# Kernel optimization log

Hardware: AMD Instinct MI355X
Metric: run time of the kernel (lower is better)

## Reference

```python
import jax, jax.numpy as jnp
import numpy as np

NUM_EXPERTS = 8
TOP_K = 2
DIM = 1024
HIDDEN = 2048
TOKENS = 8192


def setup_inputs() -> dict:
    key = jax.random.key(0)
    k0, k1, k2, k3, k4 = jax.random.split(key, 5)
    x = jax.random.normal(k0, (TOKENS, DIM), dtype=jnp.float32)
    gate_w = jax.random.normal(k1, (NUM_EXPERTS, DIM), dtype=jnp.float32) * 0.02
    # SwiGLU expert weights, stacked over experts
    w1 = jax.random.normal(k2, (NUM_EXPERTS, DIM, HIDDEN), dtype=jnp.float32) * 0.02
    w3 = jax.random.normal(k3, (NUM_EXPERTS, DIM, HIDDEN), dtype=jnp.float32) * 0.02
    w2 = jax.random.normal(k4, (NUM_EXPERTS, HIDDEN, DIM), dtype=jnp.float32) * 0.02
    return {"x": x, "gate_w": gate_w, "w1": w1, "w3": w3, "w2": w2}


def reference(x, gate_w, w1, w3, w2):
    # x: [T, D]; gate_w: [E, D]; w1,w3: [E, D, H]; w2: [E, H, D]
    E = gate_w.shape[0]
    gate_logits = x @ gate_w.T                               # [T, E]
    topk_vals, topk_idx = jax.lax.top_k(gate_logits, TOP_K)  # [T, K]
    topk_w = jax.nn.softmax(topk_vals.astype(jnp.float32), axis=-1).astype(x.dtype)
    # per-token per-expert combine weight: sum_k w[t,k] * [sel[t,k]==e]  -> [T, E]
    combine = jnp.einsum('tk,tke->te', topk_w,
                         jax.nn.one_hot(topk_idx, E, dtype=x.dtype))
    # SwiGLU experts, computed per expert over all tokens then masked-combined
    h = jnp.einsum('td,edh->eth', x, w1)                     # [E, T, H]
    g = jnp.einsum('td,edh->eth', x, w3)                     # [E, T, H]
    y = jnp.einsum('eth,ehd->etd', jax.nn.silu(h) * g, w2)   # [E, T, D]
    return jnp.einsum('te,etd->td', combine, y)              # [T, D]
```

## Files before the change

### kernel.cpp

```cpp
#include <hip/hip_runtime.h>
#include <cstdint>
#include <cstddef>

#define T_TOKENS 8192
#define DIM      1024
#define HID      2048
#define NE       8
#define HCAP     17408

typedef __attribute__((ext_vector_type(8))) short short8;
typedef __attribute__((ext_vector_type(4))) short short4v;
typedef __attribute__((ext_vector_type(4))) float f32x4;

__device__ __forceinline__ unsigned short f2bf(float f) {
  unsigned int u = __builtin_bit_cast(unsigned int, f);
  u += 0x7fffu + ((u >> 16) & 1u);
  return (unsigned short)(u >> 16);
}

__device__ __forceinline__ void gload16(const void* g, void* lds) {
  __builtin_amdgcn_global_load_lds((const __attribute__((address_space(1))) void*)g,
                                   (__attribute__((address_space(3))) void*)lds,
                                   16, 0, 0);
}

__global__ void transcvt_kernel(const float* __restrict__ in, unsigned short* __restrict__ out,
                                int K, int N) {
  __shared__ float tile[64][65];
  int e = blockIdx.z;
  int r  = threadIdx.x >> 2;
  int c0 = (threadIdx.x & 3) * 16;
  const float* src = in + ((size_t)e * K + blockIdx.y * 64 + r) * N + blockIdx.x * 64 + c0;
#pragma unroll
  for (int j = 0; j < 4; j++) {
    float4 v = *(const float4*)(src + j * 4);
    tile[r][c0 + j * 4 + 0] = v.x; tile[r][c0 + j * 4 + 1] = v.y;
    tile[r][c0 + j * 4 + 2] = v.z; tile[r][c0 + j * 4 + 3] = v.w;
  }
  __syncthreads();
  short8 o0, o1;
#pragma unroll
  for (int j = 0; j < 8; j++) o0[j] = (short)f2bf(tile[c0 + j][r]);
#pragma unroll
  for (int j = 0; j < 8; j++) o1[j] = (short)f2bf(tile[c0 + 8 + j][r]);
  unsigned short* dst = out + ((size_t)e * N + blockIdx.x * 64 + r) * K + blockIdx.y * 64 + c0;
  *(short8*)dst = o0;
  *(short8*)(dst + 8) = o1;
}

__global__ void gate_kernel(const float* __restrict__ x, const float* __restrict__ gw,
                            int2* __restrict__ sel, float2* __restrict__ wts,
                            unsigned short* __restrict__ xb) {
  int wid = threadIdx.x >> 6, lane = threadIdx.x & 63;
  int t = blockIdx.x * 4 + wid;
  const float* xr = x + (size_t)t * DIM;
  unsigned short* xo = xb + (size_t)t * DIM;
  double acc[NE];
#pragma unroll
  for (int e = 0; e < NE; e++) acc[e] = 0.0;
#pragma unroll
  for (int p = 0; p < 4; p++) {
    int idx = p * 256 + lane * 4;
    float4 xv = *(const float4*)(xr + idx);
    short4v o;
    o[0] = (short)f2bf(xv.x); o[1] = (short)f2bf(xv.y);
    o[2] = (short)f2bf(xv.z); o[3] = (short)f2bf(xv.w);
    *(short4v*)(xo + idx) = o;
#pragma unroll
    for (int e = 0; e < NE; e++) {
      float4 g = *(const float4*)(gw + e * DIM + idx);
      acc[e] += (double)xv.x * (double)g.x + (double)xv.y * (double)g.y
              + (double)xv.z * (double)g.z + (double)xv.w * (double)g.w;
    }
  }
#pragma unroll
  for (int e = 0; e < NE; e++) {
    double v = acc[e];
#pragma unroll
    for (int off = 32; off > 0; off >>= 1) v += __shfl_xor(v, off);
    acc[e] = v;
  }
  if (lane == 0) {
    float l[NE];
#pragma unroll
    for (int e = 0; e < NE; e++) l[e] = (float)acc[e];
    int i0 = 0; float v0 = l[0];
#pragma unroll
    for (int e = 1; e < NE; e++) if (l[e] > v0) { v0 = l[e]; i0 = e; }
    int i1 = -1; float v1 = -3.4e38f;
#pragma unroll
    for (int e = 0; e < NE; e++) if (e != i0 && l[e] > v1) { v1 = l[e]; i1 = e; }
    float ew = __expf(v1 - v0);
    float w0 = 1.0f / (1.0f + ew);
    float w1 = ew / (1.0f + ew);
    sel[t] = make_int2(i0, i1);
    wts[t] = make_float2(w0, w1);
  }
}

__global__ void scatter_kernel(const int2* __restrict__ sel, const float2* __restrict__ wts,
                               int* __restrict__ cnt, int* __restrict__ btok,
                               float* __restrict__ bw) {
  __shared__ int hist[NE];
  __shared__ int base[NE];
  int tid = threadIdx.x;
  if (tid < NE) hist[tid] = 0;
  __syncthreads();
  int t = blockIdx.x * 256 + tid;
  int2 s = sel[t]; float2 w = wts[t];
  int p0 = atomicAdd(&hist[s.x], 1);
  int p1 = atomicAdd(&hist[s.y], 1);
  __syncthreads();
  if (tid < NE) base[tid] = atomicAdd(&cnt[tid], hist[tid]);
  __syncthreads();
  int o0 = base[s.x] + p0;
  btok[s.x * T_TOKENS + o0] = t; bw[s.x * T_TOKENS + o0] = w.x;
  int o1 = base[s.y] + p1;
  btok[s.y * T_TOKENS + o1] = t; bw[s.y * T_TOKENS + o1] = w.y;
}

#define G1_NT (HID / 64)
#define G1_MT 64
#define G1_NWG (G1_NT * G1_MT * NE)
__global__ __launch_bounds__(256, 2) void gemm1_kernel(
    const unsigned short* __restrict__ xb, const unsigned short* __restrict__ w1t,
    const unsigned short* __restrict__ w3t, const int* __restrict__ cnt,
    const int* __restrict__ btok, const unsigned short* __restrict__ zbuf,
    unsigned short* __restrict__ h) {
  int bid = blockIdx.x;
  int wg = (bid & 7) * (G1_NWG / 8) + (bid >> 3);
  int e  = wg / (G1_NT * G1_MT);
  int rem = wg % (G1_NT * G1_MT);
  int nt = rem / G1_MT;
  int mt = rem % G1_MT;

  int cn = cnt[e];
  int pc = (cn + 127) & ~127;
  if (mt * 128 >= pc) return;
  int hoff = 0;
#pragma unroll
  for (int i = 0; i < NE; i++) { int pi = (cnt[i] + 127) & ~127; if (i < e) hoff += pi; }

  __shared__ short8 At8[1024];
  __shared__ short8 B18[512];
  __shared__ short8 B38[512];

  int tid = threadIdx.x, wid = tid >> 6, lane = tid & 63;
  int m0 = mt * 128;

  int swzcol = ((lane & 7) ^ (lane >> 3)) * 8;

  const unsigned short* asrc[4];
#pragma unroll
  for (int rd = 0; rd < 4; rd++) {
    int row = (rd * 4 + wid) * 8 + (lane >> 3);
    int r = m0 + row;
    asrc[rd] = (r < cn) ? (xb + (size_t)btok[e * T_TOKENS + r] * DIM + swzcol)
                        : (zbuf + swzcol);
  }
  const unsigned short* b1s[2]; const unsigned short* b3s[2];
#pragma unroll
  for (int rd = 0; rd < 2; rd++) {
    int row = (rd * 4 + wid) * 8 + (lane >> 3);
    size_t o = ((size_t)e * HID + nt * 64 + row) * DIM + swzcol;
    b1s[rd] = w1t + o; b3s[rd] = w3t + o;
  }

  f32x4 zero = {0.f, 0.f, 0.f, 0.f};
  f32x4 acc1[4][2], acc3[4][2];
#pragma unroll
  for (int m = 0; m < 4; m++)
#pragma unroll
    for (int n = 0; n < 2; n++) { acc1[m][n] = zero; acc3[m][n] = zero; }

  int wr = wid >> 1, wc = wid & 1;
  const char* At = (const char*)At8;
  const char* B1 = (const char*)B18;
  const char* B3 = (const char*)B38;
  int lxor = (lane & 7) << 4;

  for (int kt = 0; kt < DIM / 64; kt++) {
    int ko = kt * 64;
#pragma unroll
    for (int rd = 0; rd < 4; rd++)
      gload16(asrc[rd] + ko, (char*)At8 + (rd * 4 + wid) * 1024);
#pragma unroll
    for (int rd = 0; rd < 2; rd++) {
      gload16(b1s[rd] + ko, (char*)B18 + (rd * 4 + wid) * 1024);
      gload16(b3s[rd] + ko, (char*)B38 + (rd * 4 + wid) * 1024);
    }
    __syncthreads();
#pragma unroll
    for (int ks = 0; ks < 2; ks++) {
      int cb = (ks * 64 + (lane >> 4) * 16) ^ lxor;
      short8 a[4], f1[2], f3[2];
#pragma unroll
      for (int m = 0; m < 4; m++)
        a[m] = *(const short8*)(At + (wr * 64 + m * 16 + (lane & 15)) * 128 + cb);
#pragma unroll
      for (int n = 0; n < 2; n++) {
        int rb = (wc * 32 + n * 16 + (lane & 15)) * 128 + cb;
        f1[n] = *(const short8*)(B1 + rb);
        f3[n] = *(const short8*)(B3 + rb);
      }
#pragma unroll
      for (int m = 0; m < 4; m++)
#pragma unroll
        for (int n = 0; n < 2; n++) {
          acc1[m][n] = __builtin_amdgcn_mfma_f32_16x16x32_bf16(a[m], f1[n], acc1[m][n], 0, 0, 0);
          acc3[m][n] = __builtin_amdgcn_mfma_f32_16x16x32_bf16(a[m], f3[n], acc3[m][n], 0, 0, 0);
        }
    }
    __syncthreads();
  }

#pragma unroll
  for (int m = 0; m < 4; m++)
#pragma unroll
    for (int n = 0; n < 2; n++) {
#pragma unroll
      for (int j = 0; j < 4; j++) {
        float s1 = acc1[m][n][j], s3 = acc3[m][n][j];
        float hv = s1 / (1.0f + __expf(-s1)) * s3;
        int row = wr * 64 + m * 16 + (lane >> 4) * 4 + j;
        int col = nt * 64 + wc * 32 + n * 16 + (lane & 15);
        h[(size_t)(hoff + m0 + row) * HID + col] = f2bf(hv);
      }
    }
}

#define G2_NT (DIM / 128)
#define G2_MT 64
#define G2_NWG (G2_NT * G2_MT * NE)
__global__ __launch_bounds__(256, 2) void gemm2_kernel(
    const unsigned short* __restrict__ h, const unsigned short* __restrict__ w2t,
    const int* __restrict__ cnt, const int* __restrict__ btok,
    const float* __restrict__ bw, float* __restrict__ out) {
  int bid = blockIdx.x;
  int wg = (bid & 7) * (G2_NWG / 8) + (bid >> 3);
  int e  = wg / (G2_NT * G2_MT);
  int rem = wg % (G2_NT * G2_MT);
  int nt = rem / G2_MT;
  int mt = rem % G2_MT;

  int cn = cnt[e];
  int pc = (cn + 127) & ~127;
  if (mt * 128 >= pc) return;
  int hoff = 0;
#pragma unroll
  for (int i = 0; i < NE; i++) { int pi = (cnt[i] + 127) & ~127; if (i < e) hoff += pi; }

  __shared__ short8 At8[1024];
  __shared__ short8 Bt8[1024];

  int tid = threadIdx.x, wid = tid >> 6, lane = tid & 63;
  int m0 = mt * 128;

  int swzcol = ((lane & 7) ^ (lane >> 3)) * 8;

  const unsigned short* as[4]; const unsigned short* bs[4];
#pragma unroll
  for (int rd = 0; rd < 4; rd++) {
    int row = (rd * 4 + wid) * 8 + (lane >> 3);
    as[rd] = h + (size_t)(hoff + m0 + row) * HID + swzcol;
    bs[rd] = w2t + ((size_t)e * DIM + nt * 128 + row) * HID + swzcol;
  }

  f32x4 zero = {0.f, 0.f, 0.f, 0.f};
  f32x4 acc[4][4];
#pragma unroll
  for (int m = 0; m < 4; m++)
#pragma unroll
    for (int n = 0; n < 4; n++) acc[m][n] = zero;

  int wr = wid >> 1, wc = wid & 1;
  const char* At = (const char*)At8;
  const char* Bt = (const char*)Bt8;
  int lxor = (lane & 7) << 4;

  for (int kt = 0; kt < HID / 64; kt++) {
    int ko = kt * 64;
#pragma unroll
    for (int rd = 0; rd < 4; rd++) {
      gload16(as[rd] + ko, (char*)At8 + (rd * 4 + wid) * 1024);
      gload16(bs[rd] + ko, (char*)Bt8 + (rd * 4 + wid) * 1024);
    }
    __syncthreads();
#pragma unroll
    for (int ks = 0; ks < 2; ks++) {
      int cb = (ks * 64 + (lane >> 4) * 16) ^ lxor;
      short8 a[4], b[4];
#pragma unroll
      for (int m = 0; m < 4; m++)
        a[m] = *(const short8*)(At + (wr * 64 + m * 16 + (lane & 15)) * 128 + cb);
#pragma unroll
      for (int n = 0; n < 4; n++)
        b[n] = *(const short8*)(Bt + (wc * 64 + n * 16 + (lane & 15)) * 128 + cb);
#pragma unroll
      for (int m = 0; m < 4; m++)
#pragma unroll
        for (int n = 0; n < 4; n++)
          acc[m][n] = __builtin_amdgcn_mfma_f32_16x16x32_bf16(a[m], b[n], acc[m][n], 0, 0, 0);
    }
    __syncthreads();
  }

#pragma unroll
  for (int m = 0; m < 4; m++)
#pragma unroll
    for (int j = 0; j < 4; j++) {
      int r = m0 + wr * 64 + m * 16 + (lane >> 4) * 4 + j;
      if (r < cn) {
        int t = btok[e * T_TOKENS + r];
        float w = bw[e * T_TOKENS + r];
        size_t ob = (size_t)t * DIM + nt * 128 + wc * 64 + (lane & 15);
#pragma unroll
        for (int n = 0; n < 4; n++)
          atomicAdd(out + ob + n * 16, w * acc[m][n][j]);
      }
    }
}

extern "C" void kernel_launch(void* const* d_in, const int* in_sizes, int n_in,
                              void* d_out, int out_size, void* d_ws, size_t ws_size,
                              hipStream_t stream) {
  const float* x  = (const float*)d_in[0];
  const float* gw = (const float*)d_in[1];
  const float* w1 = (const float*)d_in[2];
  const float* w3 = (const float*)d_in[3];
  const float* w2 = (const float*)d_in[4];
  float* out = (float*)d_out;

  char* ws = (char*)d_ws;
  unsigned short* W1T = (unsigned short*)ws;
  unsigned short* W3T = W1T + (size_t)NE * HID * DIM;
  unsigned short* W2T = W3T + (size_t)NE * HID * DIM;
  unsigned short* XB  = W2T + (size_t)NE * DIM * HID;
  unsigned short* H   = XB + (size_t)T_TOKENS * DIM;
  int*   TOK = (int*)(H + (size_t)HCAP * HID);
  float* BW  = (float*)(TOK + NE * T_TOKENS);
  int*   CNT = (int*)(BW + NE * T_TOKENS);
  unsigned short* ZBUF = (unsigned short*)(CNT + 16);
  int2*   SEL = (int2*)(ZBUF + 1024);
  float2* WTS = (float2*)(SEL + T_TOKENS);

  hipMemsetAsync(d_out, 0, (size_t)out_size * sizeof(float), stream);
  hipMemsetAsync(CNT, 0, 16 * sizeof(int) + 1024 * sizeof(unsigned short), stream);

  gate_kernel<<<T_TOKENS / 4, 256, 0, stream>>>(x, gw, SEL, WTS, XB);
  scatter_kernel<<<T_TOKENS / 256, 256, 0, stream>>>(SEL, WTS, CNT, TOK, BW);
  transcvt_kernel<<<dim3(HID / 64, DIM / 64, NE), 256, 0, stream>>>(w1, W1T, DIM, HID);
  transcvt_kernel<<<dim3(HID / 64, DIM / 64, NE), 256, 0, stream>>>(w3, W3T, DIM, HID);
  transcvt_kernel<<<dim3(DIM / 64, HID / 64, NE), 256, 0, stream>>>(w2, W2T, HID, DIM);
  gemm1_kernel<<<G1_NWG, 256, 0, stream>>>(XB, W1T, W3T, CNT, TOK, ZBUF, H);
  gemm2_kernel<<<G2_NWG, 256, 0, stream>>>(H, W2T, CNT, TOK, BW, out);
}
```

Baseline: 377.3 us.

## Fuse weight transpose-convert and gating into one prep kernel; use 3D GEMM grids

Folds the three weight transpose/bf16-convert launches and the gate kernel into a single prep_kernel whose block index selects the work, cutting launch overhead and letting all of it run concurrently. The GEMM kernels drop the bid&7-based workgroup remapping (an XCD-aware swizzle) and take expert, m-tile and n-tile directly from a 3D grid. That changes dispatch order, so blocks sharing an expert's weights may spread across XCDs and lose L2 reuse.

```diff
diff --git a/kernel.cpp b/kernel.cpp
--- a/kernel.cpp
+++ b/kernel.cpp
@@ -24,13 +24,13 @@
                                    16, 0, 0);
 }
 
-__global__ void transcvt_kernel(const float* __restrict__ in, unsigned short* __restrict__ out,
-                                int K, int N) {
-  __shared__ float tile[64][65];
-  int e = blockIdx.z;
-  int r  = threadIdx.x >> 2;
-  int c0 = (threadIdx.x & 3) * 16;
-  const float* src = in + ((size_t)e * K + blockIdx.y * 64 + r) * N + blockIdx.x * 64 + c0;
+#define PREP_GATE0 12288
+__device__ __forceinline__ void transcvt_body(
+    const float* __restrict__ in, unsigned short* __restrict__ out,
+    int K, int N, int bx, int by, int e, float (*tile)[65], int tid) {
+  int r  = tid >> 2;
+  int c0 = (tid & 3) * 16;
+  const float* src = in + ((size_t)e * K + by * 64 + r) * N + bx * 64 + c0;
 #pragma unroll
   for (int j = 0; j < 4; j++) {
     float4 v = *(const float4*)(src + j * 4);
@@ -43,16 +43,38 @@
   for (int j = 0; j < 8; j++) o0[j] = (short)f2bf(tile[c0 + j][r]);
 #pragma unroll
   for (int j = 0; j < 8; j++) o1[j] = (short)f2bf(tile[c0 + 8 + j][r]);
-  unsigned short* dst = out + ((size_t)e * N + blockIdx.x * 64 + r) * K + blockIdx.y * 64 + c0;
+  unsigned short* dst = out + ((size_t)e * N + bx * 64 + r) * K + by * 64 + c0;
   *(short8*)dst = o0;
   *(short8*)(dst + 8) = o1;
 }
 
-__global__ void gate_kernel(const float* __restrict__ x, const float* __restrict__ gw,
-                            int2* __restrict__ sel, float2* __restrict__ wts,
-                            unsigned short* __restrict__ xb) {
-  int wid = threadIdx.x >> 6, lane = threadIdx.x & 63;
-  int t = blockIdx.x * 4 + wid;
+__global__ __launch_bounds__(256) void prep_kernel(
+    const float* __restrict__ x, const float* __restrict__ gw,
+    const float* __restrict__ w1, const float* __restrict__ w3,
+    const float* __restrict__ w2,
+    unsigned short* __restrict__ W1T, unsigned short* __restrict__ W3T,
+    unsigned short* __restrict__ W2T,
+    int2* __restrict__ sel, float2* __restrict__ wts,
+    unsigned short* __restrict__ xb) {
+  __shared__ float tile[64][65];
+  int bid = blockIdx.x, tid = threadIdx.x;
+
+  if (bid < PREP_GATE0) {
+    if (bid < 4096) {
+      int t = bid;
+      transcvt_body(w1, W1T, DIM, HID, t % 32, (t / 32) % 16, t / 512, tile, tid);
+    } else if (bid < 8192) {
+      int t = bid - 4096;
+      transcvt_body(w3, W3T, DIM, HID, t % 32, (t / 32) % 16, t / 512, tile, tid);
+    } else {
+      int t = bid - 8192;
+      transcvt_body(w2, W2T, HID, DIM, t % 16, (t / 16) % 32, t / 512, tile, tid);
+    }
+    return;
+  }
+
+  int wid = tid >> 6, lane = tid & 63;
+  int t = (bid - PREP_GATE0) * 4 + wid;
   const float* xr = x + (size_t)t * DIM;
   unsigned short* xo = xb + (size_t)t * DIM;
   double acc[NE];
@@ -92,9 +114,9 @@
     for (int e = 0; e < NE; e++) if (e != i0 && l[e] > v1) { v1 = l[e]; i1 = e; }
     float ew = __expf(v1 - v0);
     float w0 = 1.0f / (1.0f + ew);
-    float w1 = ew / (1.0f + ew);
+    float w1v = ew / (1.0f + ew);
     sel[t] = make_int2(i0, i1);
-    wts[t] = make_float2(w0, w1);
+    wts[t] = make_float2(w0, w1v);
   }
 }
 
@@ -119,27 +141,20 @@
   btok[s.y * T_TOKENS + o1] = t; bw[s.y * T_TOKENS + o1] = w.y;
 }
 
-#define G1_NT (HID / 64)
-#define G1_MT 64
-#define G1_NWG (G1_NT * G1_MT * NE)
 __global__ __launch_bounds__(256, 2) void gemm1_kernel(
     const unsigned short* __restrict__ xb, const unsigned short* __restrict__ w1t,
     const unsigned short* __restrict__ w3t, const int* __restrict__ cnt,
     const int* __restrict__ btok, const unsigned short* __restrict__ zbuf,
     unsigned short* __restrict__ h) {
-  int bid = blockIdx.x;
-  int wg = (bid & 7) * (G1_NWG / 8) + (bid >> 3);
-  int e  = wg / (G1_NT * G1_MT);
-  int rem = wg % (G1_NT * G1_MT);
-  int nt = rem / G1_MT;
-  int mt = rem % G1_MT;
-
+  int e = blockIdx.z;
   int cn = cnt[e];
   int pc = (cn + 127) & ~127;
+  int mt = blockIdx.y;
   if (mt * 128 >= pc) return;
   int hoff = 0;
 #pragma unroll
   for (int i = 0; i < NE; i++) { int pi = (cnt[i] + 127) & ~127; if (i < e) hoff += pi; }
+  int nt = blockIdx.x;
 
   __shared__ short8 At8[1024];
   __shared__ short8 B18[512];
@@ -229,26 +244,19 @@
     }
 }
 
-#define G2_NT (DIM / 128)
-#define G2_MT 64
-#define G2_NWG (G2_NT * G2_MT * NE)
 __global__ __launch_bounds__(256, 2) void gemm2_kernel(
     const unsigned short* __restrict__ h, const unsigned short* __restrict__ w2t,
     const int* __restrict__ cnt, const int* __restrict__ btok,
     const float* __restrict__ bw, float* __restrict__ out) {
-  int bid = blockIdx.x;
-  int wg = (bid & 7) * (G2_NWG / 8) + (bid >> 3);
-  int e  = wg / (G2_NT * G2_MT);
-  int rem = wg % (G2_NT * G2_MT);
-  int nt = rem / G2_MT;
-  int mt = rem % G2_MT;
-
+  int e = blockIdx.z;
   int cn = cnt[e];
   int pc = (cn + 127) & ~127;
+  int mt = blockIdx.y;
   if (mt * 128 >= pc) return;
   int hoff = 0;
 #pragma unroll
   for (int i = 0; i < NE; i++) { int pi = (cnt[i] + 127) & ~127; if (i < e) hoff += pi; }
+  int nt = blockIdx.x;
 
   __shared__ short8 At8[1024];
   __shared__ short8 Bt8[1024];
@@ -347,11 +355,8 @@
   hipMemsetAsync(d_out, 0, (size_t)out_size * sizeof(float), stream);
   hipMemsetAsync(CNT, 0, 16 * sizeof(int) + 1024 * sizeof(unsigned short), stream);
 
-  gate_kernel<<<T_TOKENS / 4, 256, 0, stream>>>(x, gw, SEL, WTS, XB);
+  prep_kernel<<<14336, 256, 0, stream>>>(x, gw, w1, w3, w2, W1T, W3T, W2T, SEL, WTS, XB);
   scatter_kernel<<<T_TOKENS / 256, 256, 0, stream>>>(SEL, WTS, CNT, TOK, BW);
-  transcvt_kernel<<<dim3(HID / 64, DIM / 64, NE), 256, 0, stream>>>(w1, W1T, DIM, HID);
-  transcvt_kernel<<<dim3(HID / 64, DIM / 64, NE), 256, 0, stream>>>(w3, W3T, DIM, HID);
-  transcvt_kernel<<<dim3(DIM / 64, HID / 64, NE), 256, 0, stream>>>(w2, W2T, HID, DIM);
-  gemm1_kernel<<<G1_NWG, 256, 0, stream>>>(XB, W1T, W3T, CNT, TOK, ZBUF, H);
-  gemm2_kernel<<<G2_NWG, 256, 0, stream>>>(H, W2T, CNT, TOK, BW, out);
-}
+  gemm1_kernel<<<dim3(HID / 64, 64, NE), 256, 0, stream>>>(XB, W1T, W3T, CNT, TOK, ZBUF, H);
+  gemm2_kernel<<<dim3(DIM / 128, 64, NE), 256, 0, stream>>>(H, W2T, CNT, TOK, BW, out);
+}
```

Measured after the change: 357.4 us. -5.3%, faster.
